# Performance work log

Hardware: AMD Instinct MI355X
Metric: run time of the kernel (lower is better)

## Reference

```python
import jax, jax.numpy as jnp
import numpy as np

M, N, D = 512, 4096, 128
H = N // D  # 32
L = 4096   # cache length


def setup_inputs() -> dict:
    key = jax.random.key(0)
    ks = jax.random.split(key, 6)
    s = 1.0 / np.sqrt(N)
    return {
        "X": jax.random.normal(ks[0], (M, N), jnp.float32),
        "W_q": jax.random.normal(ks[1], (N, N), jnp.float32) * s,
        "W_k": jax.random.normal(ks[2], (N, N), jnp.float32) * s,
        "W_v": jax.random.normal(ks[3], (N, N), jnp.float32) * s,
        "cache_K": jax.random.normal(ks[4], (H, L, D), jnp.float32),
        "cache_V": jax.random.normal(ks[5], (H, L, D), jnp.float32),
        "P": 3584,
    }


def reference(X, W_q, W_k, W_v, cache_K, cache_V, P):
    # nn.Linear(N, N, bias=False): y = x @ W.T
    q = (X @ W_q.T).reshape(M, H, D).transpose(1, 0, 2)  # [H, M, D]
    k = (X @ W_k.T).reshape(M, H, D).transpose(1, 0, 2)  # [H, M, D]
    v = (X @ W_v.T).reshape(M, H, D).transpose(1, 0, 2)  # [H, M, D]
    # KV-cache write at position P (static slice under jit for fixed P)
    cK = jax.lax.dynamic_update_slice(cache_K, k, (0, P, 0))  # [H, L, D]
    cV = jax.lax.dynamic_update_slice(cache_V, v, (0, P, 0))
    # attention over the full cache, no 1/sqrt(D) scaling (faithful to source)
    scores = jnp.einsum("hmd,hld->hml", q, cK)   # [H, M, L]
    weights = jax.nn.softmax(scores, axis=-1)
    out = jnp.einsum("hml,hld->hmd", weights, cV)  # [H, M, D]
    return out.transpose(1, 0, 2).reshape(M, H * D)  # [M, N]
```

## Files before the change

### kernel.cpp

```cpp
#include <hip/hip_runtime.h>
#include <hip/hip_fp16.h>

typedef _Float16 f16x8 __attribute__((ext_vector_type(8)));
typedef float    f32x4 __attribute__((ext_vector_type(4)));

#define MFMA16(a,b,c) __builtin_amdgcn_mfma_f32_16x16x32_f16(a,b,c,0,0,0)

__device__ __forceinline__ void gload_lds16(const void* g, void* l) {
  __builtin_amdgcn_global_load_lds(
      (const __attribute__((address_space(1))) void*)g,
      (__attribute__((address_space(3))) void*)l, 16, 0, 0);
}

__global__ void cvt_f32_f16(const float* __restrict__ src,
                            _Float16* __restrict__ dst, int n8) {
  int i = blockIdx.x * blockDim.x + threadIdx.x;
  int stride = gridDim.x * blockDim.x;
  for (; i < n8; i += stride) {
    const float4* s = (const float4*)src + 2 * (size_t)i;
    float4 a = s[0], b = s[1];
    f16x8 o;
    o[0]=(_Float16)a.x; o[1]=(_Float16)a.y; o[2]=(_Float16)a.z; o[3]=(_Float16)a.w;
    o[4]=(_Float16)b.x; o[5]=(_Float16)b.y; o[6]=(_Float16)b.z; o[7]=(_Float16)b.w;
    ((f16x8*)dst)[i] = o;
  }
}

__global__ __launch_bounds__(256) void qkv_gemm_fused(
    const _Float16* __restrict__ X,
    const float* __restrict__ Wq,
    const float* __restrict__ Wk,
    const float* __restrict__ Wv,
    const float* __restrict__ cK,
    const float* __restrict__ cV,
    _Float16* __restrict__ Q16,
    _Float16* __restrict__ Kc,
    _Float16* __restrict__ Vt16,
    const int* __restrict__ Pp)
{
  __shared__ __align__(16) _Float16 smem[(128 + 64) * 64];
  _Float16* As = smem;
  _Float16* Bs = smem + 128 * 64;
  const int bid = blockIdx.x;
  const int tid = threadIdx.x;

  if (bid < 768) {
    const int xcd = bid & 7, s = bid >> 3;
    const int nt = xcd * 24 + (s >> 2);
    const int mt = s & 3;
    const int m0 = mt * 128, n0 = nt * 64;
    const int wave = tid >> 6, lane = tid & 63;
    const int g = lane >> 4, c = lane & 15;
    const int wr = wave >> 1, wc = wave & 1;
    const float* Wp = (n0 < 4096) ? Wq : ((n0 < 8192) ? Wk : Wv);
    const int n0l = n0 & 4095;
    const int ar  = lane >> 3;
    const int acs = (lane & 7) * 16;
    const int brow = tid >> 2;
    const int bc32 = (tid & 3) * 16;
    const float* wsrc = Wp + (size_t)(n0l + brow) * 4096 + bc32;
    const int bsw = (brow & 7) << 4;
    float4 breg[4];
#pragma unroll
    for (int i = 0; i < 4; i++) breg[i] = *(const float4*)(wsrc + i * 4);

    f32x4 acc[4][2] = {};
    for (int k0 = 0; k0 < 4096; k0 += 64) {
      __syncthreads();
#pragma unroll
      for (int p = 0; p < 4; p++) {
        int chunk = wave * 4 + p;
        int row = chunk * 8 + ar;
        gload_lds16((const char*)(X + (size_t)(m0 + row) * 4096 + k0) + (acs ^ ((row & 7) << 4)),
                    (char*)As + chunk * 1024);
      }
      {
        const float* bv = (const float*)breg;
        f16x8 h0, h1;
#pragma unroll
        for (int i = 0; i < 8; i++) { h0[i] = (_Float16)bv[i]; h1[i] = (_Float16)bv[8 + i]; }
        char* rb = (char*)Bs + brow * 128;
        *(f16x8*)(rb + (((tid & 3) * 32)      ^ bsw)) = h0;
        *(f16x8*)(rb + (((tid & 3) * 32 + 16) ^ bsw)) = h1;
      }
      __syncthreads();
      if (k0 + 64 < 4096) {
        const float* ns = wsrc + k0 + 64;
#pragma unroll
        for (int i = 0; i < 4; i++) breg[i] = *(const float4*)(ns + i * 4);
      }
      f16x8 af[2][4], bf[2][2];
#pragma unroll
      for (int mi = 0; mi < 4; mi++) {
        int row = wr * 64 + mi * 16 + c;
        int sw = (row & 7) << 4;
#pragma unroll
        for (int kc = 0; kc < 2; kc++)
          af[kc][mi] = *(const f16x8*)((const char*)As + row * 128 + ((kc * 64 + g * 16) ^ sw));
      }
#pragma unroll
      for (int ni = 0; ni < 2; ni++) {
        int row = wc * 32 + ni * 16 + c;
        int sw = (row & 7) << 4;
#pragma unroll
        for (int kc = 0; kc < 2; kc++)
          bf[kc][ni] = *(const f16x8*)((const char*)Bs + row * 128 + ((kc * 64 + g * 16) ^ sw));
      }
#pragma unroll
      for (int kc = 0; kc < 2; kc++)
#pragma unroll
        for (int mi = 0; mi < 4; mi++)
#pragma unroll
          for (int ni = 0; ni < 2; ni++)
            acc[mi][ni] = MFMA16(af[kc][mi], bf[kc][ni], acc[mi][ni]);
    }
    const int p = Pp[0];
    const int wsel = n0 >> 12;
    const int h = (n0 & 4095) >> 7;
    const int dbase = n0 & 127;
#pragma unroll
    for (int mi = 0; mi < 4; mi++) {
#pragma unroll
      for (int ni = 0; ni < 2; ni++) {
#pragma unroll
        for (int j = 0; j < 4; j++) {
          int m = m0 + wr * 64 + mi * 16 + 4 * g + j;
          int d = dbase + wc * 32 + ni * 16 + c;
          _Float16 hv = (_Float16)acc[mi][ni][j];
          if (wsel == 0)      Q16[(size_t)(h * 512 + m) * 128 + d] = hv;
          else if (wsel == 1) Kc[(size_t)(h * 4096 + p + m) * 128 + d] = hv;
          else                Vt16[((size_t)h * 128 + d) * 4096 + p + m] = hv;
        }
      }
    }
    return;
  }

  const int p = Pp[0];
  const int cb = bid - 768;
  if (cb < 512) {
    const int total = 32 * 4096 * 16;
    const int stride = 512 * 256;
    for (int i = cb * 256 + tid; i < total; i += stride) {
      int l = (i >> 4) & 4095;
      if ((unsigned)(l - p) < 512u) continue;
      const float4* s = (const float4*)cK + 2 * (size_t)i;
      float4 a = s[0], b = s[1];
      f16x8 o;
      o[0]=(_Float16)a.x; o[1]=(_Float16)a.y; o[2]=(_Float16)a.z; o[3]=(_Float16)a.w;
      o[4]=(_Float16)b.x; o[5]=(_Float16)b.y; o[6]=(_Float16)b.z; o[7]=(_Float16)b.w;
      ((f16x8*)Kc)[i] = o;
    }
  } else {
    _Float16 (*t)[74] = (_Float16 (*)[74])smem;
    const int r = tid >> 4, c4 = (tid & 15) * 4;
    const int d = tid >> 2, lc = (tid & 3) * 16;
#pragma unroll
    for (int rep = 0; rep < 2; rep++) {
      int b = (cb - 512) * 2 + rep;
      int h = b >> 7, rest = b & 127;
      int lt = rest >> 1, dt = rest & 1;
      int l0 = lt * 64, d0 = dt * 64;
      __syncthreads();
#pragma unroll
      for (int i = 0; i < 4; i++) {
        int l = r + i * 16;
        float4 v = *(const float4*)&cV[((size_t)h * 4096 + l0 + l) * 128 + d0 + c4];
        t[c4 + 0][l] = (_Float16)v.x;
        t[c4 + 1][l] = (_Float16)v.y;
        t[c4 + 2][l] = (_Float16)v.z;
        t[c4 + 3][l] = (_Float16)v.w;
      }
      __syncthreads();
#pragma unroll
      for (int i = 0; i < 2; i++) {
        int l = l0 + lc + i * 8;
        if ((unsigned)(l - p) < 512u) continue;
        f16x8 o = *(const f16x8*)&t[d][lc + i * 8];
        *(f16x8*)&Vt16[((size_t)h * 128 + d0 + d) * 4096 + l] = o;
      }
    }
  }
}

__global__ __launch_bounds__(512, 2) void attn_part(
    const _Float16* __restrict__ Q16,
    const _Float16* __restrict__ Kc,
    const _Float16* __restrict__ Vt,
    float* __restrict__ Opart,
    float* __restrict__ Mpart,
    float* __restrict__ Lpart)
{
  __shared__ __align__(16) _Float16 Ks[64 * 128];
  __shared__ __align__(16) _Float16 Vs[128 * 64];
  __shared__ __align__(16) _Float16 Pl[8][16][68];
  const int bid = blockIdx.x;
  const int xcd = bid & 7, s = bid >> 3;
  const int group = xcd * 16 + (s >> 2);
  const int mt = s & 3;
  const int ls = group >> 5, h = group & 31;
  const int m0 = mt * 128;
  const int tid = threadIdx.x, wave = tid >> 6, lane = tid & 63;
  const int g = lane >> 4, c = lane & 15;
  const int mw = m0 + wave * 16;
  const _Float16* Kh  = Kc + (size_t)h * 4096 * 128;
  const _Float16* Vth = Vt + (size_t)h * 128 * 4096;
  f16x8 qf[4];
#pragma unroll
  for (int kc = 0; kc < 4; kc++)
    qf[kc] = *(const f16x8*)&Q16[(size_t)(h * 512 + mw + c) * 128 + kc * 32 + g * 8];
  f32x4 o[8] = {};
  float mrow[4] = {-3e38f, -3e38f, -3e38f, -3e38f};
  float lrow[4] = {0.f, 0.f, 0.f, 0.f};
  const int klr = lane >> 4, klb = (lane & 15) * 16;
  const int vlr = lane >> 3, vlb = (lane & 7) * 16;

  const int l_begin = ls * 1024;
  for (int l0 = l_begin; l0 < l_begin + 1024; l0 += 64) {
    __syncthreads();
#pragma unroll
    for (int p = 0; p < 2; p++) {
      int chunk = p * 8 + wave;
      int kr = chunk * 4 + klr;
      gload_lds16((const char*)Kh + (size_t)(l0 + kr) * 256 + (klb ^ ((kr & 7) << 4)),
                  (char*)Ks + chunk * 1024);
      int vd = chunk * 8 + vlr;
      gload_lds16((const char*)Vth + (size_t)vd * 8192 + (size_t)l0 * 2 + (vlb ^ ((vd & 7) << 4)),
                  (char*)Vs + chunk * 1024);
    }
    __syncthreads();
    f32x4 sc[4] = {};
#pragma unroll
    for (int ni = 0; ni < 4; ni++) {
      int kr = ni * 16 + c;
      f16x8 kf[4];
#pragma unroll
      for (int kc = 0; kc < 4; kc++)
        kf[kc] = *(const f16x8*)((const char*)Ks + kr * 256 + ((kc * 64 + g * 16) ^ ((kr & 7) << 4)));
#pragma unroll
      for (int kc = 0; kc < 4; kc++)
        sc[ni] = MFMA16(qf[kc], kf[kc], sc[ni]);
    }
    float scale[4];
#pragma unroll
    for (int j = 0; j < 4; j++) {
      float tm = sc[0][j];
#pragma unroll
      for (int ni = 1; ni < 4; ni++) tm = fmaxf(tm, sc[ni][j]);
      tm = fmaxf(tm, __shfl_xor(tm, 1, 64));
      tm = fmaxf(tm, __shfl_xor(tm, 2, 64));
      tm = fmaxf(tm, __shfl_xor(tm, 4, 64));
      tm = fmaxf(tm, __shfl_xor(tm, 8, 64));
      float mn = fmaxf(mrow[j], tm);
      scale[j] = __expf(mrow[j] - mn);
      mrow[j] = mn;
    }
    float rs[4] = {0.f, 0.f, 0.f, 0.f};
#pragma unroll
    for (int ni = 0; ni < 4; ni++) {
#pragma unroll
      for (int j = 0; j < 4; j++) {
        float pv = __expf(sc[ni][j] - mrow[j]);
        sc[ni][j] = pv;
        rs[j] += pv;
      }
    }
#pragma unroll
    for (int j = 0; j < 4; j++) {
      rs[j] += __shfl_xor(rs[j], 1, 64);
      rs[j] += __shfl_xor(rs[j], 2, 64);
      rs[j] += __shfl_xor(rs[j], 4, 64);
      rs[j] += __shfl_xor(rs[j], 8, 64);
      lrow[j] = lrow[j] * scale[j] + rs[j];
    }
#pragma unroll
    for (int dn = 0; dn < 8; dn++)
#pragma unroll
      for (int j = 0; j < 4; j++) o[dn][j] *= scale[j];
#pragma unroll
    for (int ni = 0; ni < 4; ni++)
#pragma unroll
      for (int j = 0; j < 4; j++)
        Pl[wave][4 * g + j][ni * 16 + c] = (_Float16)sc[ni][j];
    f16x8 pa[2];
#pragma unroll
    for (int kc = 0; kc < 2; kc++)
      pa[kc] = *(const f16x8*)&Pl[wave][c][kc * 32 + g * 8];
#pragma unroll
    for (int dn = 0; dn < 8; dn++) {
      int vr = dn * 16 + c;
#pragma unroll
      for (int kc = 0; kc < 2; kc++) {
        f16x8 vb = *(const f16x8*)((const char*)Vs + vr * 128 + ((kc * 64 + g * 16) ^ ((vr & 7) << 4)));
        o[dn] = MFMA16(pa[kc], vb, o[dn]);
      }
    }
  }
  const size_t pbase = ((size_t)(ls * 32 + h) * 512);
#pragma unroll
  for (int dn = 0; dn < 8; dn++) {
#pragma unroll
    for (int j = 0; j < 4; j++) {
      int m = mw + 4 * g + j;
      Opart[(pbase + m) * 128 + dn * 16 + c] = o[dn][j];
    }
  }
  if (c == 0) {
#pragma unroll
    for (int j = 0; j < 4; j++) {
      int m = mw + 4 * g + j;
      Mpart[pbase + m] = mrow[j];
      Lpart[pbase + m] = lrow[j];
    }
  }
}

__global__ __launch_bounds__(256) void attn_combine(
    const float* __restrict__ Opart,
    const float* __restrict__ Mpart,
    const float* __restrict__ Lpart,
    float* __restrict__ out)
{
  int idx = blockIdx.x * 256 + threadIdx.x;
  int row = idx >> 5;
  int d4  = idx & 31;
  int h = row >> 9, m = row & 511;
  float Ms[4];
  float mx = -3e38f;
#pragma unroll
  for (int s = 0; s < 4; s++) {
    Ms[s] = Mpart[(size_t)(s * 32 + h) * 512 + m];
    mx = fmaxf(mx, Ms[s]);
  }
  float lsum = 0.f;
  float4 acc = make_float4(0.f, 0.f, 0.f, 0.f);
#pragma unroll
  for (int s = 0; s < 4; s++) {
    float w = __expf(Ms[s] - mx);
    lsum += w * Lpart[(size_t)(s * 32 + h) * 512 + m];
    float4 ov = ((const float4*)(Opart + ((size_t)(s * 32 + h) * 512 + m) * 128))[d4];
    acc.x += w * ov.x; acc.y += w * ov.y; acc.z += w * ov.z; acc.w += w * ov.w;
  }
  float inv = 1.f / lsum;
  float4 r = make_float4(acc.x * inv, acc.y * inv, acc.z * inv, acc.w * inv);
  *(float4*)&out[(size_t)m * 4096 + h * 128 + d4 * 4] = r;
}

extern "C" void kernel_launch(void* const* d_in, const int* in_sizes, int n_in,
                              void* d_out, int out_size, void* d_ws, size_t ws_size,
                              hipStream_t stream) {
  const float* X  = (const float*)d_in[0];
  const float* Wq = (const float*)d_in[1];
  const float* Wk = (const float*)d_in[2];
  const float* Wv = (const float*)d_in[3];
  const float* cK = (const float*)d_in[4];
  const float* cV = (const float*)d_in[5];
  const int*   Pp = (const int*)d_in[6];
  float* out = (float*)d_out;

  char* ws = (char*)d_ws;
  _Float16* X16  = (_Float16*)(ws);
  float* Opart = (float*)(ws + ((size_t)4  << 20));
  float* Mpart = (float*)(ws + ((size_t)36 << 20));
  float* Lpart = (float*)(ws + ((size_t)37 << 20));
  _Float16* Q16  = (_Float16*)(ws + ((size_t)100 << 20));
  _Float16* K16  = (_Float16*)(ws + ((size_t)104 << 20));
  _Float16* V16t = (_Float16*)(ws + ((size_t)136 << 20));

  cvt_f32_f16<<<dim3(1024), dim3(256), 0, stream>>>(X, X16, 512 * 4096 / 8);
  qkv_gemm_fused<<<dim3(768 + 512 + 2048), dim3(256), 0, stream>>>(
      X16, Wq, Wk, Wv, cK, cV, Q16, K16, V16t, Pp);
  attn_part<<<dim3(512), dim3(512), 0, stream>>>(Q16, K16, V16t, Opart, Mpart, Lpart);
  attn_combine<<<dim3(2048), dim3(256), 0, stream>>>(Opart, Mpart, Lpart, out);
}
```

Before: 228.9 us.

## Double-buffer LDS tiles in fused QKV GEMM with one barrier per step

The QKV projection GEMM now uses two LDS buffers for the A (X) and B (weight) tiles. Each step writes the next B tile and issues async global-to-LDS loads for the next A tile while the MFMAs consume the current buffer, which drops one of the two barriers per iteration. It also adds a min-blocks-per-CU hint of 3 to the launch bounds. LDS use per block doubles and the occupancy hint may force register limits. The last iterations issue extra wrapped-around loads that are never used.

New measurement: 221.7 us. 3.1% less time.

```diff
diff --git a/kernel.cpp b/kernel.cpp
--- a/kernel.cpp
+++ b/kernel.cpp
@@ -26,7 +26,7 @@
   }
 }
 
-__global__ __launch_bounds__(256) void qkv_gemm_fused(
+__global__ __launch_bounds__(256, 3) void qkv_gemm_fused(
     const _Float16* __restrict__ X,
     const float* __restrict__ Wq,
     const float* __restrict__ Wk,
@@ -38,9 +38,9 @@
     _Float16* __restrict__ Vt16,
     const int* __restrict__ Pp)
 {
-  __shared__ __align__(16) _Float16 smem[(128 + 64) * 64];
+  __shared__ __align__(16) _Float16 smem[2 * (128 + 64) * 64];
   _Float16* As = smem;
-  _Float16* Bs = smem + 128 * 64;
+  _Float16* Bs = smem + 2 * 128 * 64;
   const int bid = blockIdx.x;
   const int tid = threadIdx.x;
 
@@ -60,35 +60,46 @@
     const int bc32 = (tid & 3) * 16;
     const float* wsrc = Wp + (size_t)(n0l + brow) * 4096 + bc32;
     const int bsw = (brow & 7) << 4;
+
     float4 breg[4];
-#pragma unroll
-    for (int i = 0; i < 4; i++) breg[i] = *(const float4*)(wsrc + i * 4);
-
-    f32x4 acc[4][2] = {};
-    for (int k0 = 0; k0 < 4096; k0 += 64) {
-      __syncthreads();
+    auto loadB = [&](int k0) {
+      const float* ns = wsrc + k0;
+#pragma unroll
+      for (int i = 0; i < 4; i++) breg[i] = *(const float4*)(ns + i * 4);
+    };
+    auto writeB = [&](int buf) {
+      const float* bv = (const float*)breg;
+      f16x8 h0, h1;
+#pragma unroll
+      for (int i = 0; i < 8; i++) { h0[i] = (_Float16)bv[i]; h1[i] = (_Float16)bv[8 + i]; }
+      char* rb = (char*)Bs + buf * 8192 + brow * 128;
+      *(f16x8*)(rb + (((tid & 3) * 32)      ^ bsw)) = h0;
+      *(f16x8*)(rb + (((tid & 3) * 32 + 16) ^ bsw)) = h1;
+    };
+    auto stageA = [&](int k0, int buf) {
 #pragma unroll
       for (int p = 0; p < 4; p++) {
         int chunk = wave * 4 + p;
         int row = chunk * 8 + ar;
         gload_lds16((const char*)(X + (size_t)(m0 + row) * 4096 + k0) + (acs ^ ((row & 7) << 4)),
-                    (char*)As + chunk * 1024);
-      }
-      {
-        const float* bv = (const float*)breg;
-        f16x8 h0, h1;
-#pragma unroll
-        for (int i = 0; i < 8; i++) { h0[i] = (_Float16)bv[i]; h1[i] = (_Float16)bv[8 + i]; }
-        char* rb = (char*)Bs + brow * 128;
-        *(f16x8*)(rb + (((tid & 3) * 32)      ^ bsw)) = h0;
-        *(f16x8*)(rb + (((tid & 3) * 32 + 16) ^ bsw)) = h1;
-      }
-      __syncthreads();
-      if (k0 + 64 < 4096) {
-        const float* ns = wsrc + k0 + 64;
-#pragma unroll
-        for (int i = 0; i < 4; i++) breg[i] = *(const float4*)(ns + i * 4);
-      }
+                    (char*)As + buf * 16384 + chunk * 1024);
+      }
+    };
+
+    f32x4 acc[4][2] = {};
+    loadB(0);
+    writeB(0);
+    stageA(0, 0);
+    loadB(64);
+    __syncthreads();
+
+    for (int t = 0; t < 64; ++t) {
+      const int cur = t & 1, nxt = cur ^ 1;
+      writeB(nxt);
+      loadB(((t + 2) & 63) << 6);
+      stageA(((t + 1) & 63) << 6, nxt);
+      const char* Ab = (const char*)As + cur * 16384;
+      const char* Bb = (const char*)Bs + cur * 8192;
       f16x8 af[2][4], bf[2][2];
 #pragma unroll
       for (int mi = 0; mi < 4; mi++) {
@@ -96,7 +107,7 @@
         int sw = (row & 7) << 4;
 #pragma unroll
         for (int kc = 0; kc < 2; kc++)
-          af[kc][mi] = *(const f16x8*)((const char*)As + row * 128 + ((kc * 64 + g * 16) ^ sw));
+          af[kc][mi] = *(const f16x8*)(Ab + row * 128 + ((kc * 64 + g * 16) ^ sw));
       }
 #pragma unroll
       for (int ni = 0; ni < 2; ni++) {
@@ -104,7 +115,7 @@
         int sw = (row & 7) << 4;
 #pragma unroll
         for (int kc = 0; kc < 2; kc++)
-          bf[kc][ni] = *(const f16x8*)((const char*)Bs + row * 128 + ((kc * 64 + g * 16) ^ sw));
+          bf[kc][ni] = *(const f16x8*)(Bb + row * 128 + ((kc * 64 + g * 16) ^ sw));
       }
 #pragma unroll
       for (int kc = 0; kc < 2; kc++)
@@ -113,7 +124,9 @@
 #pragma unroll
           for (int ni = 0; ni < 2; ni++)
             acc[mi][ni] = MFMA16(af[kc][mi], bf[kc][ni], acc[mi][ni]);
-    }
+      __syncthreads();
+    }
+
     const int p = Pp[0];
     const int wsel = n0 >> 12;
     const int h = (n0 & 4095) >> 7;
```
